# Kernel optimization log

Measured on AMD Instinct MI355X. Metric: run time of the kernel, lower is better.

Reference implementation:

```python
import jax, jax.numpy as jnp
import numpy as np

HEADS = 16
DIM_HEAD = 64
SCALE = DIM_HEAD ** -0.5


def setup_inputs() -> dict:
    key = jax.random.key(0)
    k1, k2, k3, k4 = jax.random.split(key, 4)
    b, n, dim = 2, 2048, 1024
    inner = HEADS * DIM_HEAD
    x = jax.random.normal(k1, (b, n, dim), dtype=jnp.float32)
    mask = jax.random.randint(k2, (b, n), 0, 2, dtype=jnp.int32)
    w_qkv = jax.random.normal(k3, (3 * inner, dim), dtype=jnp.float32) * (dim ** -0.5)
    w_out = jax.random.normal(k4, (dim, inner), dtype=jnp.float32) * (inner ** -0.5)
    return {"x": x, "mask": mask, "w_qkv": w_qkv, "w_out": w_out}


def reference(x, mask, w_qkv, w_out):
    b, n, dim = x.shape
    # qkv projection (no bias), split into q,k,v and reshape b n (h d) -> b h n d
    qkv = jnp.einsum('bnd,ed->bne', x, w_qkv)
    q, k, v = jnp.split(qkv, 3, axis=-1)
    def to_heads(t):
        return t.reshape(b, n, HEADS, DIM_HEAD).transpose(0, 2, 1, 3)
    q, k, v = to_heads(q), to_heads(k), to_heads(v)
    # scores [b,h,n,n]
    dots = jnp.einsum('bhid,bhjd->bhij', q, k) * SCALE
    # pairwise mask: mask_i * mask_j, broadcast over heads
    pair = (mask[:, :, None] * mask[:, None, :])[:, None, :, :]  # [b,1,n,n]
    neg = -jnp.finfo(dots.dtype).max
    dots = jnp.where(pair == 0, neg, dots)
    attn = jax.nn.softmax(dots, axis=-1)
    out = jnp.einsum('bhij,bhjd->bhid', attn, v)
    out = out.transpose(0, 2, 1, 3).reshape(b, n, HEADS * DIM_HEAD)
    return jnp.einsum('bne,de->bnd', out, w_out)
```

## Files before the change

### kernel.cpp

```cpp
#include <hip/hip_runtime.h>
#include <stdint.h>

typedef unsigned short u16;
typedef uint32_t u32;
typedef __attribute__((ext_vector_type(8))) short bf8;
typedef __attribute__((ext_vector_type(4))) float f4;
typedef __attribute__((ext_vector_type(16))) float f16f;
typedef __attribute__((ext_vector_type(4))) unsigned short us4;

__device__ __forceinline__ u16 f2bf(float f) {
    uint32_t u = __float_as_uint(f);
    u += 0x7FFF + ((u >> 16) & 1);
    return (u16)(u >> 16);
}
__device__ __forceinline__ float bf2f(u16 v) {
    return __uint_as_float(((uint32_t)v) << 16);
}
__device__ __forceinline__ void gld_lds16(const u16* g, u16* l) {
    __builtin_amdgcn_global_load_lds(
        (const __attribute__((address_space(1))) void*)g,
        (__attribute__((address_space(3))) void*)l, 16, 0, 0);
}
__device__ __forceinline__ f16f mfma32(bf8 a, bf8 b, f16f c) {
    return __builtin_amdgcn_mfma_f32_32x32x16_bf16(a, b, c, 0, 0, 0);
}
__device__ __forceinline__ u32 cvtpk(float lo, float hi) {
    u32 r; asm("v_cvt_pk_bf16_f32 %0, %1, %2" : "=v"(r) : "v"(lo), "v"(hi)); return r;
}
__device__ __forceinline__ void plswap(u32& a, u32& b) {
    asm("v_permlane32_swap_b32 %0, %1" : "+v"(a), "+v"(b));
}
__device__ __forceinline__ float fexp2(float x) {
    float r; asm("v_exp_f32 %0, %1" : "=v"(r) : "v"(x)); return r;
}

struct alignas(8) US4 { u16 a, b, c, d; };

__global__ void cvt_all(const float* __restrict__ x, const float* __restrict__ wqkv,
                        const float* __restrict__ wout,
                        u16* __restrict__ xbf, u16* __restrict__ wqkvbf, u16* __restrict__ woutbf) {
    int i = blockIdx.x * blockDim.x + threadIdx.x;
    const float* src; u16* dst; int off;
    if (i < 1048576)      { src = x;    dst = xbf;    off = i; }
    else if (i < 1835008) { src = wqkv; dst = wqkvbf; off = i - 1048576; }
    else                  { src = wout; dst = woutbf; off = i - 1835008; }
    float4 v = ((const float4*)src)[off];
    US4 o; o.a = f2bf(v.x); o.b = f2bf(v.y); o.c = f2bf(v.z); o.d = f2bf(v.w);
    ((US4*)dst)[off] = o;
}

__global__ __launch_bounds__(256)
void gemm_qkv(const u16* __restrict__ A, const u16* __restrict__ W,
              u16* __restrict__ Qo, u16* __restrict__ Ko, u16* __restrict__ Vo)
{
    __shared__ __align__(16) u16 lsmem[2 * 128 * 64];
    u16* lA = lsmem;
    u16* lB = lsmem + 128 * 64;
    const int tid = threadIdx.x;
    const int lane = tid & 63, wid = tid >> 6;
    const int g = lane >> 4, c = lane & 15;
    const int bid = blockIdx.x;
    const int wg = (bid & 7) * 96 + (bid >> 3);
    const int m0 = (wg / 24) * 128, n0 = (wg % 24) * 128;
    const int wr = wid >> 1, wc = wid & 1;

    f4 acc[4][4];
#pragma unroll
    for (int i = 0; i < 4; ++i)
#pragma unroll
        for (int j = 0; j < 4; ++j) { acc[i][j][0] = 0.f; acc[i][j][1] = 0.f; acc[i][j][2] = 0.f; acc[i][j][3] = 0.f; }

    for (int k0 = 0; k0 < 1024; k0 += 64) {
        __syncthreads();
#pragma unroll
        for (int i = 0; i < 4; ++i) {
            int chunk = i * 256 + tid;
            int row = chunk >> 3, cc = chunk & 7;
            int gc = cc ^ (row & 7);
            gld_lds16(A + (m0 + row) * 1024 + k0 + gc * 8, lA + (i * 256 + wid * 64) * 8);
            gld_lds16(W + (n0 + row) * 1024 + k0 + gc * 8, lB + (i * 256 + wid * 64) * 8);
        }
        __syncthreads();
#pragma unroll
        for (int kk = 0; kk < 2; ++kk) {
            bf8 af[4], bfr[4];
#pragma unroll
            for (int mi = 0; mi < 4; ++mi) {
                int row = wr * 64 + mi * 16 + c;
                af[mi] = *(const bf8*)&lA[row * 64 + ((kk * 4 + g) ^ (row & 7)) * 8];
            }
#pragma unroll
            for (int ni = 0; ni < 4; ++ni) {
                int row = wc * 64 + ni * 16 + c;
                bfr[ni] = *(const bf8*)&lB[row * 64 + ((kk * 4 + g) ^ (row & 7)) * 8];
            }
#pragma unroll
            for (int mi = 0; mi < 4; ++mi)
#pragma unroll
                for (int ni = 0; ni < 4; ++ni)
                    acc[mi][ni] = __builtin_amdgcn_mfma_f32_16x16x32_bf16(af[mi], bfr[ni], acc[mi][ni], 0, 0, 0);
        }
    }

    __syncthreads();
    u16* eb = lsmem + wid * 4096;
    const int e0 = n0 + wc * 64;
    const int part = e0 >> 10;
    const int hh = (e0 & 1023) >> 6;
    const float scale = (part == 0) ? 0.18033688011112042f : 1.0f;

    if (part < 2) {
#pragma unroll
        for (int mi = 0; mi < 4; ++mi)
#pragma unroll
            for (int ni = 0; ni < 4; ++ni) {
                int colL = ni * 16 + c;
#pragma unroll
                for (int r = 0; r < 4; ++r) {
                    int tokL = mi * 16 + g * 4 + r;
                    int chk = ((colL >> 3) ^ (tokL & 7));
                    eb[tokL * 64 + chk * 8 + (colL & 7)] = f2bf(acc[mi][ni][r] * scale);
                }
            }
        u16* dst0 = (part == 0) ? Qo : Ko;
#pragma unroll
        for (int i = 0; i < 8; ++i) {
            int row = i * 8 + (lane >> 3);
            int ch = lane & 7;
            bf8 v = *(const bf8*)&eb[row * 64 + ((ch ^ (row & 7)) << 3)];
            int tok = m0 + wr * 64 + row;
            int bb = tok >> 11, nn = tok & 2047;
            *(bf8*)&dst0[((bb * 16 + hh) * 2048 + nn) * 64 + ch * 8] = v;
        }
    } else {
#pragma unroll
        for (int mi = 0; mi < 4; ++mi)
#pragma unroll
            for (int ni = 0; ni < 4; ++ni) {
                int dL = ni * 16 + c;
                int tokL0 = mi * 16 + g * 4;
                int tchk = ((tokL0 >> 3) ^ (dL & 7));
                us4 w;
                w[0] = f2bf(acc[mi][ni][0]); w[1] = f2bf(acc[mi][ni][1]);
                w[2] = f2bf(acc[mi][ni][2]); w[3] = f2bf(acc[mi][ni][3]);
                *(us4*)&eb[dL * 64 + tchk * 8 + (tokL0 & 7)] = w;
            }
#pragma unroll
        for (int i = 0; i < 8; ++i) {
            int dr = i * 8 + (lane >> 3);
            int ch = lane & 7;
            bf8 v = *(const bf8*)&eb[dr * 64 + ((ch ^ (dr & 7)) << 3)];
            int tok0 = m0 + wr * 64 + ch * 8;
            int bb = tok0 >> 11, nn = tok0 & 2047;
            *(bf8*)&Vo[((bb * 16 + hh) * 64 + dr) * 2048 + nn] = v;
        }
    }
}

__global__ void vmean_kernel(const u16* __restrict__ VT, float* __restrict__ vmean) {
    int bh = blockIdx.x;
    int tid = threadIdx.x;
    int d = tid >> 2, seg = tid & 3;
    const u16* row = VT + bh * 131072 + d * 2048 + seg * 512;
    float s = 0.f;
    for (int i = 0; i < 512; i += 8) {
        bf8 v = *(const bf8*)&row[i];
#pragma unroll
        for (int j = 0; j < 8; ++j) s += bf2f((u16)v[j]);
    }
    __shared__ float red[256];
    red[tid] = s;
    __syncthreads();
    if (seg == 0)
        vmean[bh * 64 + d] = (red[tid] + red[tid + 1] + red[tid + 2] + red[tid + 3]) * (1.0f / 2048.0f);
}

__global__ __launch_bounds__(512, 4)
void attn_kernel(const u16* __restrict__ Q, const u16* __restrict__ K, const u16* __restrict__ VT,
                 const int* __restrict__ mask, const float* __restrict__ vmean,
                 u16* __restrict__ O)
{
    __shared__ __align__(16) u16 lS[2][2][8192];
    __shared__ u16 lBias[2048];

    const int tid = threadIdx.x;
    const int lane = tid & 63, wid = tid >> 6;
    const int q = lane & 31, hi = lane >> 5;
    const int half = wid >> 2, qw = wid & 3;
    const int B = blockIdx.x;
    const int xcd = B & 7, idx = B >> 3;
    const int bh = xcd * 4 + (idx & 3), qt = idx >> 2;
    const int b = bh >> 4, h = bh & 15;
    const u16* Qb = Q + bh * (2048 * 64);
    const u16* Kb = K + bh * (2048 * 64);
    const u16* Vb = VT + bh * (64 * 2048);

    const u16 NEGB = f2bf(-1e30f);
    for (int i = tid; i < 2048; i += 512)
        lBias[i] = mask[b * 2048 + i] ? (u16)0 : NEGB;

    const int qrow = qt * 128 + qw * 32 + q;
    bf8 qf[4];
#pragma unroll
    for (int s = 0; s < 4; ++s)
        qf[s] = *(const bf8*)&Qb[qrow * 64 + s * 16 + hi * 8];

    f16f oacc[2];
#pragma unroll
    for (int i = 0; i < 16; ++i) { oacc[0][i] = 0.f; oacc[1][i] = 0.f; }
    float mrun = 20.0f, lrun = 0.f;

    bf8 oneb;
#pragma unroll
    for (int i = 0; i < 8; ++i) oneb[i] = 0;
    if (hi == 0) oneb[0] = (short)0x3F80;

    const int sl = tid & 255;
    const int r0 = sl >> 3,         c0 = (sl & 7) ^ (r0 & 7);
    const int r1 = (sl + 256) >> 3, c1 = ((sl + 256) & 7) ^ (r1 & 7);
    const int tile0 = half * 16;

    {
        u16* bp = &lS[half][0][0];
        gld_lds16(Kb + (tile0 * 64 + r0) * 64 + c0 * 8, bp + sl * 8);
        gld_lds16(Kb + (tile0 * 64 + r1) * 64 + c1 * 8, bp + (sl + 256) * 8);
        gld_lds16(Vb + r0 * 2048 + tile0 * 64 + c0 * 8, bp + 4096 + sl * 8);
        gld_lds16(Vb + r1 * 2048 + tile0 * 64 + c1 * 8, bp + 4096 + (sl + 256) * 8);
    }
    __syncthreads();

    for (int t = 0; t < 16; ++t) {
        const int cur = t & 1;
        if (t < 15) {
            const int tn = tile0 + t + 1;
            u16* bn = &lS[half][cur ^ 1][0];
            gld_lds16(Kb + (tn * 64 + r0) * 64 + c0 * 8, bn + sl * 8);
            gld_lds16(Kb + (tn * 64 + r1) * 64 + c1 * 8, bn + (sl + 256) * 8);
            gld_lds16(Vb + r0 * 2048 + tn * 64 + c0 * 8, bn + 4096 + sl * 8);
            gld_lds16(Vb + r1 * 2048 + tn * 64 + c1 * 8, bn + 4096 + (sl + 256) * 8);
        }
        const u16* kbuf = &lS[half][cur][0];
        const u16* vbuf = kbuf + 4096;
        const int tt = tile0 + t;

        f16f st[2];
        __builtin_amdgcn_s_setprio(1);
#pragma unroll
        for (int kb = 0; kb < 2; ++kb) {
            bf8 ba;
#pragma unroll
            for (int i = 0; i < 8; ++i) ba[i] = 0;
            if (hi == 0) ba[0] = (short)lBias[tt * 64 + kb * 32 + q];
            f16f z;
#pragma unroll
            for (int i = 0; i < 16; ++i) z[i] = 0.f;
            st[kb] = mfma32(ba, oneb, z);
            const int row = kb * 32 + q;
#pragma unroll
            for (int s = 0; s < 4; ++s) {
                bf8 kf = *(const bf8*)&kbuf[row * 64 + (((2 * s + hi) ^ (row & 7)) << 3)];
                st[kb] = mfma32(kf, qf[s], st[kb]);
            }
        }
        __builtin_amdgcn_s_setprio(0);

        float tx[16];
#pragma unroll
        for (int i = 0; i < 16; ++i) tx[i] = fmaxf(st[0][i], st[1][i]);
#pragma unroll
        for (int i = 0; i < 8; ++i) tx[i] = fmaxf(tx[i], tx[i + 8]);
#pragma unroll
        for (int i = 0; i < 4; ++i) tx[i] = fmaxf(tx[i], tx[i + 4]);
        float tm = fmaxf(fmaxf(tx[0], tx[1]), fmaxf(tx[2], tx[3]));
        tm = fmaxf(tm, __shfl_xor(tm, 32));

        if (!__all(tm <= mrun + 8.0f)) {
            float mnew = fmaxf(mrun, tm);
            float al = fexp2(mrun - mnew);
            mrun = mnew;
            lrun *= al;
#pragma unroll
            for (int i = 0; i < 16; ++i) { oacc[0][i] *= al; oacc[1][i] *= al; }
        }
#pragma unroll
        for (int kb = 0; kb < 2; ++kb)
#pragma unroll
            for (int i = 0; i < 16; ++i)
                st[kb][i] = fexp2(st[kb][i] - mrun);
        float sx[16];
#pragma unroll
        for (int i = 0; i < 16; ++i) sx[i] = st[0][i] + st[1][i];
#pragma unroll
        for (int i = 0; i < 8; ++i) sx[i] += sx[i + 8];
#pragma unroll
        for (int i = 0; i < 4; ++i) sx[i] += sx[i + 4];
        float ts = (sx[0] + sx[1]) + (sx[2] + sx[3]);
        ts += __shfl_xor(ts, 32);
        lrun += ts;

        bf8 pa[4];
#pragma unroll
        for (int kb = 0; kb < 2; ++kb)
#pragma unroll
            for (int gp = 0; gp < 2; ++gp) {
                u32 a0 = cvtpk(st[kb][gp * 8 + 0], st[kb][gp * 8 + 1]);
                u32 a1 = cvtpk(st[kb][gp * 8 + 2], st[kb][gp * 8 + 3]);
                u32 b0 = cvtpk(st[kb][gp * 8 + 4], st[kb][gp * 8 + 5]);
                u32 b1 = cvtpk(st[kb][gp * 8 + 6], st[kb][gp * 8 + 7]);
                plswap(a0, b0);
                plswap(a1, b1);
                union { bf8 v; u32 u[4]; } pu;
                pu.u[0] = a0; pu.u[1] = a1; pu.u[2] = b0; pu.u[3] = b1;
                pa[kb * 2 + gp] = pu.v;
            }

        __builtin_amdgcn_s_setprio(1);
#pragma unroll
        for (int db = 0; db < 2; ++db) {
            const int vrow = db * 32 + q;
#pragma unroll
            for (int s = 0; s < 4; ++s) {
                bf8 vf = *(const bf8*)&vbuf[vrow * 64 + (((2 * s + hi) ^ (vrow & 7)) << 3)];
                oacc[db] = mfma32(vf, pa[s], oacc[db]);
            }
        }
        __builtin_amdgcn_s_setprio(0);
        __syncthreads();
    }

    float* mb = (float*)&lS[0][0][0];
    float* mp = mb + (qw * 64 + lane) * 35;
    if (half == 1) {
        mp[0] = mrun; mp[1] = lrun;
#pragma unroll
        for (int i = 0; i < 16; ++i) { mp[2 + i] = oacc[0][i]; mp[18 + i] = oacc[1][i]; }
    }
    __syncthreads();
    if (half == 0) {
        float m2 = mp[0], l2 = mp[1];
        float mm = fmaxf(mrun, m2);
        float e1 = fexp2(mrun - mm), e2 = fexp2(m2 - mm);
        float inv = 1.0f / (lrun * e1 + l2 * e2);
        float a1 = e1 * inv, a2 = e2 * inv;
        u16* eb = ((u16*)&lS[0][0][0]) + 20480 + qw * 2432;
#pragma unroll
        for (int db = 0; db < 2; ++db)
#pragma unroll
            for (int q2 = 0; q2 < 4; ++q2) {
                us4 w;
#pragma unroll
                for (int j = 0; j < 4; ++j) {
                    int i = q2 * 4 + j;
                    w[j] = f2bf(oacc[db][i] * a1 + mp[2 + db * 16 + i] * a2);
                }
                *(us4*)&eb[q * 76 + db * 32 + q2 * 8 + hi * 4] = w;
            }
#pragma unroll
        for (int i = 0; i < 4; ++i) {
            int row = i * 8 + (lane >> 3);
            int ch = lane & 7;
            bf8 v = *(const bf8*)&eb[row * 76 + ch * 8];
            int tok = qt * 128 + qw * 32 + row;
            if (lBias[tok] != 0) {
                const float* vm = vmean + bh * 64 + ch * 8;
                float4 v0 = ((const float4*)vm)[0];
                float4 v1 = ((const float4*)vm)[1];
                v[0] = (short)f2bf(v0.x); v[1] = (short)f2bf(v0.y);
                v[2] = (short)f2bf(v0.z); v[3] = (short)f2bf(v0.w);
                v[4] = (short)f2bf(v1.x); v[5] = (short)f2bf(v1.y);
                v[6] = (short)f2bf(v1.z); v[7] = (short)f2bf(v1.w);
            }
            *(bf8*)&O[(b * 2048 + tok) * 1024 + h * 64 + ch * 8] = v;
        }
    }
}

__global__ __launch_bounds__(256)
void gemm_out(const u16* __restrict__ A, const u16* __restrict__ W, float* __restrict__ out)
{
    __shared__ __align__(16) u16 lA[128 * 64];
    __shared__ __align__(16) u16 lB[128 * 64];
    const int tid = threadIdx.x;
    const int lane = tid & 63, wid = tid >> 6;
    const int g = lane >> 4, c = lane & 15;
    const int bid = blockIdx.x;
    const int wg = (bid & 7) * 32 + (bid >> 3);
    const int m0 = (wg >> 3) * 128, n0 = (wg & 7) * 128;
    const int wr = wid >> 1, wc = wid & 1;

    f4 acc[4][4];
#pragma unroll
    for (int i = 0; i < 4; ++i)
#pragma unroll
        for (int j = 0; j < 4; ++j) { acc[i][j][0] = 0.f; acc[i][j][1] = 0.f; acc[i][j][2] = 0.f; acc[i][j][3] = 0.f; }

    for (int k0 = 0; k0 < 1024; k0 += 64) {
        __syncthreads();
#pragma unroll
        for (int i = 0; i < 4; ++i) {
            int chunk = i * 256 + tid;
            int row = chunk >> 3, cc = chunk & 7;
            int gc = cc ^ (row & 7);
            gld_lds16(A + (m0 + row) * 1024 + k0 + gc * 8, lA + (i * 256 + wid * 64) * 8);
            gld_lds16(W + (n0 + row) * 1024 + k0 + gc * 8, lB + (i * 256 + wid * 64) * 8);
        }
        __syncthreads();
#pragma unroll
        for (int kk = 0; kk < 2; ++kk) {
            bf8 af[4], bfr[4];
#pragma unroll
            for (int mi = 0; mi < 4; ++mi) {
                int row = wr * 64 + mi * 16 + c;
                af[mi] = *(const bf8*)&lA[row * 64 + ((kk * 4 + g) ^ (row & 7)) * 8];
            }
#pragma unroll
            for (int ni = 0; ni < 4; ++ni) {
                int row = wc * 64 + ni * 16 + c;
                bfr[ni] = *(const bf8*)&lB[row * 64 + ((kk * 4 + g) ^ (row & 7)) * 8];
            }
#pragma unroll
            for (int mi = 0; mi < 4; ++mi)
#pragma unroll
                for (int ni = 0; ni < 4; ++ni)
                    acc[mi][ni] = __builtin_amdgcn_mfma_f32_16x16x32_bf16(af[mi], bfr[ni], acc[mi][ni], 0, 0, 0);
        }
    }
#pragma unroll
    for (int mi = 0; mi < 4; ++mi) {
        int row0 = m0 + wr * 64 + mi * 16 + g * 4;
#pragma unroll
        for (int ni = 0; ni < 4; ++ni) {
            int col = n0 + wc * 64 + ni * 16 + c;
#pragma unroll
            for (int r = 0; r < 4; ++r)
                out[(row0 + r) * 1024 + col] = acc[mi][ni][r];
        }
    }
}

extern "C" void kernel_launch(void* const* d_in, const int* in_sizes, int n_in,
                              void* d_out, int out_size, void* d_ws, size_t ws_size,
                              hipStream_t stream) {
    const float* x    = (const float*)d_in[0];
    const int*   mask = (const int*)d_in[1];
    const float* wqkv = (const float*)d_in[2];
    const float* wout = (const float*)d_in[3];
    float* out = (float*)d_out;

    u16* ws = (u16*)d_ws;
    u16* xbf    = ws;
    u16* wqkvbf = xbf + 4096 * 1024;
    u16* woutbf = wqkvbf + 3072 * 1024;
    u16* qb     = woutbf + 1024 * 1024;
    u16* kb     = qb + 2 * 16 * 2048 * 64;
    u16* vtb    = kb + 2 * 16 * 2048 * 64;
    float* vmean = (float*)(vtb + 2 * 16 * 2048 * 64);
    u16* ob = xbf;

    cvt_all<<<8192, 256, 0, stream>>>(x, wqkv, wout, xbf, wqkvbf, woutbf);
    gemm_qkv<<<768, 256, 0, stream>>>(xbf, wqkvbf, qb, kb, vtb);
    vmean_kernel<<<32, 256, 0, stream>>>(vtb, vmean);
    attn_kernel<<<512, 512, 0, stream>>>(qb, kb, vtb, mask, vmean, ob);
    gemm_out<<<256, 256, 0, stream>>>(ob, woutbf, out);
}
```

Before: 138.5 us.

## Split attention into 32-query blocks with four-way KV split and direct global loads

The attention kernel now uses 256-thread blocks, each handling 32 query rows. Its four waves each process one quarter of the KV sequence (8 tiles) and are merged with a four-way softmax combine through LDS. The LDS double-buffered K/V staging and the per-block bias array are gone: K and V fragments and the mask are read directly from global memory. The aim is more blocks for occupancy and no barriers inside the loop, at the cost of losing shared-memory reuse of K/V across query waves, so global and L2 traffic rises by about four times.

```diff
diff --git a/kernel.cpp b/kernel.cpp
--- a/kernel.cpp
+++ b/kernel.cpp
@@ -175,18 +175,17 @@
         vmean[bh * 64 + d] = (red[tid] + red[tid + 1] + red[tid + 2] + red[tid + 3]) * (1.0f / 2048.0f);
 }
 
-__global__ __launch_bounds__(512, 4)
+__global__ __launch_bounds__(256, 4)
 void attn_kernel(const u16* __restrict__ Q, const u16* __restrict__ K, const u16* __restrict__ VT,
                  const int* __restrict__ mask, const float* __restrict__ vmean,
                  u16* __restrict__ O)
 {
-    __shared__ __align__(16) u16 lS[2][2][8192];
-    __shared__ u16 lBias[2048];
+    __shared__ __align__(16) float msc[3 * 64 * 34];
+    __shared__ __align__(16) u16 ebuf[32 * 76];
 
     const int tid = threadIdx.x;
     const int lane = tid & 63, wid = tid >> 6;
     const int q = lane & 31, hi = lane >> 5;
-    const int half = wid >> 2, qw = wid & 3;
     const int B = blockIdx.x;
     const int xcd = B & 7, idx = B >> 3;
     const int bh = xcd * 4 + (idx & 3), qt = idx >> 2;
@@ -194,12 +193,10 @@
     const u16* Qb = Q + bh * (2048 * 64);
     const u16* Kb = K + bh * (2048 * 64);
     const u16* Vb = VT + bh * (64 * 2048);
-
+    const int* mk = mask + b * 2048;
     const u16 NEGB = f2bf(-1e30f);
-    for (int i = tid; i < 2048; i += 512)
-        lBias[i] = mask[b * 2048 + i] ? (u16)0 : NEGB;
-
-    const int qrow = qt * 128 + qw * 32 + q;
+
+    const int qrow = qt * 32 + q;
     bf8 qf[4];
 #pragma unroll
     for (int s = 0; s < 4; ++s)
@@ -215,54 +212,31 @@
     for (int i = 0; i < 8; ++i) oneb[i] = 0;
     if (hi == 0) oneb[0] = (short)0x3F80;
 
-    const int sl = tid & 255;
-    const int r0 = sl >> 3,         c0 = (sl & 7) ^ (r0 & 7);
-    const int r1 = (sl + 256) >> 3, c1 = ((sl + 256) & 7) ^ (r1 & 7);
-    const int tile0 = half * 16;
-
-    {
-        u16* bp = &lS[half][0][0];
-        gld_lds16(Kb + (tile0 * 64 + r0) * 64 + c0 * 8, bp + sl * 8);
-        gld_lds16(Kb + (tile0 * 64 + r1) * 64 + c1 * 8, bp + (sl + 256) * 8);
-        gld_lds16(Vb + r0 * 2048 + tile0 * 64 + c0 * 8, bp + 4096 + sl * 8);
-        gld_lds16(Vb + r1 * 2048 + tile0 * 64 + c1 * 8, bp + 4096 + (sl + 256) * 8);
-    }
-    __syncthreads();
-
-    for (int t = 0; t < 16; ++t) {
-        const int cur = t & 1;
-        if (t < 15) {
-            const int tn = tile0 + t + 1;
-            u16* bn = &lS[half][cur ^ 1][0];
-            gld_lds16(Kb + (tn * 64 + r0) * 64 + c0 * 8, bn + sl * 8);
-            gld_lds16(Kb + (tn * 64 + r1) * 64 + c1 * 8, bn + (sl + 256) * 8);
-            gld_lds16(Vb + r0 * 2048 + tn * 64 + c0 * 8, bn + 4096 + sl * 8);
-            gld_lds16(Vb + r1 * 2048 + tn * 64 + c1 * 8, bn + 4096 + (sl + 256) * 8);
-        }
-        const u16* kbuf = &lS[half][cur][0];
-        const u16* vbuf = kbuf + 4096;
-        const int tt = tile0 + t;
+    const u16* vp0 = Vb + q * 2048 + hi * 8;
+    const u16* vp1 = Vb + (32 + q) * 2048 + hi * 8;
+
+    for (int t = 0; t < 8; ++t) {
+        const int tt = wid * 8 + t;
 
         f16f st[2];
-        __builtin_amdgcn_s_setprio(1);
 #pragma unroll
         for (int kb = 0; kb < 2; ++kb) {
+            const int kvrow = tt * 64 + kb * 32 + q;
             bf8 ba;
 #pragma unroll
             for (int i = 0; i < 8; ++i) ba[i] = 0;
-            if (hi == 0) ba[0] = (short)lBias[tt * 64 + kb * 32 + q];
+            if (hi == 0) ba[0] = (short)(mk[kvrow] ? (u16)0 : NEGB);
             f16f z;
 #pragma unroll
             for (int i = 0; i < 16; ++i) z[i] = 0.f;
             st[kb] = mfma32(ba, oneb, z);
-            const int row = kb * 32 + q;
+            const u16* kp = Kb + kvrow * 64 + hi * 8;
 #pragma unroll
             for (int s = 0; s < 4; ++s) {
-                bf8 kf = *(const bf8*)&kbuf[row * 64 + (((2 * s + hi) ^ (row & 7)) << 3)];
+                bf8 kf = *(const bf8*)&kp[s * 16];
                 st[kb] = mfma32(kf, qf[s], st[kb]);
             }
         }
-        __builtin_amdgcn_s_setprio(0);
 
         float tx[16];
 #pragma unroll
@@ -314,54 +288,65 @@
                 pa[kb * 2 + gp] = pu.v;
             }
 
-        __builtin_amdgcn_s_setprio(1);
-#pragma unroll
-        for (int db = 0; db < 2; ++db) {
-            const int vrow = db * 32 + q;
-#pragma unroll
-            for (int s = 0; s < 4; ++s) {
-                bf8 vf = *(const bf8*)&vbuf[vrow * 64 + (((2 * s + hi) ^ (vrow & 7)) << 3)];
-                oacc[db] = mfma32(vf, pa[s], oacc[db]);
-            }
-        }
-        __builtin_amdgcn_s_setprio(0);
-        __syncthreads();
-    }
-
-    float* mb = (float*)&lS[0][0][0];
-    float* mp = mb + (qw * 64 + lane) * 35;
-    if (half == 1) {
+        const u16* v0 = vp0 + tt * 64;
+        const u16* v1 = vp1 + tt * 64;
+#pragma unroll
+        for (int s = 0; s < 4; ++s) {
+            bf8 vf = *(const bf8*)&v0[s * 16];
+            oacc[0] = mfma32(vf, pa[s], oacc[0]);
+        }
+#pragma unroll
+        for (int s = 0; s < 4; ++s) {
+            bf8 vf = *(const bf8*)&v1[s * 16];
+            oacc[1] = mfma32(vf, pa[s], oacc[1]);
+        }
+    }
+
+    if (wid != 0) {
+        float* mp = msc + ((wid - 1) * 64 + lane) * 34;
         mp[0] = mrun; mp[1] = lrun;
 #pragma unroll
         for (int i = 0; i < 16; ++i) { mp[2 + i] = oacc[0][i]; mp[18 + i] = oacc[1][i]; }
     }
     __syncthreads();
-    if (half == 0) {
-        float m2 = mp[0], l2 = mp[1];
-        float mm = fmaxf(mrun, m2);
-        float e1 = fexp2(mrun - mm), e2 = fexp2(m2 - mm);
-        float inv = 1.0f / (lrun * e1 + l2 * e2);
-        float a1 = e1 * inv, a2 = e2 * inv;
-        u16* eb = ((u16*)&lS[0][0][0]) + 20480 + qw * 2432;
-#pragma unroll
-        for (int db = 0; db < 2; ++db)
-#pragma unroll
-            for (int q2 = 0; q2 < 4; ++q2) {
-                us4 w;
-#pragma unroll
-                for (int j = 0; j < 4; ++j) {
-                    int i = q2 * 4 + j;
-                    w[j] = f2bf(oacc[db][i] * a1 + mp[2 + db * 16 + i] * a2);
-                }
-                *(us4*)&eb[q * 76 + db * 32 + q2 * 8 + hi * 4] = w;
-            }
+    if (wid == 0) {
+        const float* p1 = msc + (0 * 64 + lane) * 34;
+        const float* p2 = msc + (1 * 64 + lane) * 34;
+        const float* p3 = msc + (2 * 64 + lane) * 34;
+        float m1 = p1[0], l1 = p1[1];
+        float m2 = p2[0], l2 = p2[1];
+        float m3 = p3[0], l3 = p3[1];
+        float mm = fmaxf(fmaxf(mrun, m1), fmaxf(m2, m3));
+        float e0 = fexp2(mrun - mm), e1 = fexp2(m1 - mm), e2 = fexp2(m2 - mm), e3 = fexp2(m3 - mm);
+        float inv = 1.0f / (lrun * e0 + l1 * e1 + l2 * e2 + l3 * e3);
+        float a0 = e0 * inv, a1 = e1 * inv, a2 = e2 * inv, a3 = e3 * inv;
+        float ov0[16], ov1[16];
+#pragma unroll
+        for (int i = 0; i < 16; ++i) {
+            ov0[i] = oacc[0][i] * a0 + p1[2 + i] * a1 + p2[2 + i] * a2 + p3[2 + i] * a3;
+            ov1[i] = oacc[1][i] * a0 + p1[18 + i] * a1 + p2[18 + i] * a2 + p3[18 + i] * a3;
+        }
+#pragma unroll
+        for (int q2 = 0; q2 < 4; ++q2) {
+            us4 w;
+#pragma unroll
+            for (int j = 0; j < 4; ++j) w[j] = f2bf(ov0[q2 * 4 + j]);
+            *(us4*)&ebuf[q * 76 + q2 * 8 + hi * 4] = w;
+        }
+#pragma unroll
+        for (int q2 = 0; q2 < 4; ++q2) {
+            us4 w;
+#pragma unroll
+            for (int j = 0; j < 4; ++j) w[j] = f2bf(ov1[q2 * 4 + j]);
+            *(us4*)&ebuf[q * 76 + 32 + q2 * 8 + hi * 4] = w;
+        }
 #pragma unroll
         for (int i = 0; i < 4; ++i) {
             int row = i * 8 + (lane >> 3);
             int ch = lane & 7;
-            bf8 v = *(const bf8*)&eb[row * 76 + ch * 8];
-            int tok = qt * 128 + qw * 32 + row;
-            if (lBias[tok] != 0) {
+            bf8 v = *(const bf8*)&ebuf[row * 76 + ch * 8];
+            int tok = qt * 32 + row;
+            if (mk[tok] == 0) {
                 const float* vm = vmean + bh * 64 + ch * 8;
                 float4 v0 = ((const float4*)vm)[0];
                 float4 v1 = ((const float4*)vm)[1];
@@ -460,6 +445,6 @@
     cvt_all<<<8192, 256, 0, stream>>>(x, wqkv, wout, xbf, wqkvbf, woutbf);
     gemm_qkv<<<768, 256, 0, stream>>>(xbf, wqkvbf, qb, kb, vtb);
     vmean_kernel<<<32, 256, 0, stream>>>(vtb, vmean);
-    attn_kernel<<<512, 512, 0, stream>>>(qb, kb, vtb, mask, vmean, ob);
+    attn_kernel<<<2048, 256, 0, stream>>>(qb, kb, vtb, mask, vmean, ob);
     gemm_out<<<256, 256, 0, stream>>>(ob, woutbf, out);
 }
```

New measurement: 209.1 us. 50.9% more time.
